# Optimization experiments

Hardware: AMD Instinct MI355X
Metric: run time of the kernel (lower is better)

## Reference

```python
import jax, jax.numpy as jnp
import numpy as np

N_EXPERTS = 8  # matches init n_experts


def _dispatch(x, expert_weights, top_experts, bias):
    """Faithful port of Experts.forward: sort tokens by expert, binned_gather
    into [E, capacity, d] with capacity-based token dropping, binned_scatter
    back weighted by expert_weights, then add bias. (The shown source never
    applies self.expert inside permute_and_compute, so the expert compute is
    identity; cond/mask are gathered then discarded and do not affect output.)"""
    b, n, d = x.shape
    top_k = top_experts.shape[-1]
    T = b * n * top_k
    # expert_capacity = int(top_k * tokens / n_experts)  (static)
    C = (top_k * b * n) // N_EXPERTS
    te = top_experts.reshape(-1).astype(jnp.int32)          # [T]
    w = expert_weights.reshape(-1)                           # [T]
    # ops.sort (stable radix sort over expert ids)
    order = jnp.argsort(te, stable=True)                     # indices [T]
    bin_ids = te[order]                                      # sorted expert ids
    # ops.histogram + inclusive_cumsum -> bin starts
    tpe = jnp.zeros((N_EXPERTS,), jnp.int32).at[te].add(1)   # tokens_per_expert
    starts = jnp.cumsum(tpe) - tpe                           # exclusive cumsum
    pos = jnp.arange(T, dtype=jnp.int32) - starts[bin_ids]   # position in bin
    valid = pos < C                                          # capacity drop
    slot = bin_ids * C + pos                                 # flat [E*C] slot
    tok = order // top_k                                     # source token row
    xf = x.reshape(-1, d)
    # binned_gather: [E*C, d], invalid entries routed to a dummy row
    gathered = (jnp.zeros((N_EXPERTS * C + 1, d), x.dtype)
                .at[jnp.where(valid, slot, N_EXPERTS * C)].set(xf[tok]))[:N_EXPERTS * C]
    # binned_scatter: out[tok] += w * gathered[slot] for valid entries
    wv = jnp.where(valid, w[order], jnp.zeros((), w.dtype))
    out = (jnp.zeros((b * n, d), x.dtype)
           .at[tok].add(wv[:, None] * gathered[jnp.where(valid, slot, 0)]))
    return out.reshape(b, n, d) + bias


def setup_inputs() -> dict:
    key = jax.random.key(0)
    k = jax.random.split(key, 6)
    b, n, d, dc, top_k = 4, 4096, 1024, 256, 2
    x = jax.random.normal(k[0], (b, n, d), jnp.float32)
    cond = jax.random.normal(k[1], (b, n, dc), jnp.float32)
    mask = jnp.ones((b, n), jnp.bool_)
    scores = jax.random.uniform(k[2], (b, n, N_EXPERTS), jnp.float32)
    expert_weights = jax.random.uniform(k[3], (b, n, top_k), jnp.float32)
    top_experts = jax.random.randint(k[4], (b, n, top_k), 0, N_EXPERTS, jnp.int32)
    bias = jax.random.normal(k[5], (d,), jnp.float32)
    return {"x": x, "cond": cond, "mask": mask, "scores": scores,
            "expert_weights": expert_weights, "top_experts": top_experts,
            "bias": bias}


def reference(x, cond, mask, scores, expert_weights, top_experts, bias):
    return _dispatch(x, expert_weights, top_experts, bias)
```

## Files before the change

### kernel.cpp

```cpp
#include <hip/hip_runtime.h>

#define N_EXPERTS 8
#define ROWS_PB 8
#define ENT_PB 16
typedef unsigned long long u64;
typedef float f32x4 __attribute__((ext_vector_type(4)));
typedef int i32x4 __attribute__((ext_vector_type(4)));

__device__ __forceinline__ void packed_add(u64& c0, u64& c1, int e) {
  if (e < 4) c0 += 1ull << (16 * e);
  else       c1 += 1ull << (16 * (e - 4));
}
__device__ __forceinline__ void packed_add_val(u64& c0, u64& c1, int e, int v) {
  if (e < 4) c0 += (u64)v << (16 * e);
  else       c1 += (u64)v << (16 * (e - 4));
}
__device__ __forceinline__ int packed_get(u64 c0, u64 c1, int e) {
  return (e < 4) ? (int)((c0 >> (16 * e)) & 0xFFFF)
                 : (int)((c1 >> (16 * (e - 4))) & 0xFFFF);
}

__global__ __launch_bounds__(256) void hist_kernel(
    const int* __restrict__ te, int* __restrict__ hist) {
  __shared__ u64 w0s[4], w1s[4];
  const int tid = threadIdx.x;
  const int lane = tid & 63, wid = tid >> 6;
  const int g = blockIdx.x * 256 + tid;
  const i32x4 v = reinterpret_cast<const i32x4*>(te)[g];

  u64 c0 = 0, c1 = 0;
  packed_add(c0, c1, v.x & 7);
  packed_add(c0, c1, v.y & 7);
  packed_add(c0, c1, v.z & 7);
  packed_add(c0, c1, v.w & 7);
#pragma unroll
  for (int m = 1; m < 64; m <<= 1) {
    c0 += __shfl_xor(c0, m);
    c1 += __shfl_xor(c1, m);
  }
  if (lane == 0) { w0s[wid] = c0; w1s[wid] = c1; }
  __syncthreads();
  if (tid < N_EXPERTS) {
    int s = 0;
#pragma unroll
    for (int ww = 0; ww < 4; ++ww) s += packed_get(w0s[ww], w1s[ww], tid);
    hist[blockIdx.x * N_EXPERTS + tid] = s;
  }
}

__global__ __launch_bounds__(256) void fused_kernel(
    const float* __restrict__ x, const int* __restrict__ te,
    const float* __restrict__ ew, const int* __restrict__ hist,
    const float* __restrict__ bias, float* __restrict__ out, int C) {
  __shared__ u64 w0s[4], w1s[4];
  __shared__ float scale_s[ROWS_PB];
  const int tid = threadIdx.x;
  const int lane = tid & 63, wid = tid >> 6;
  const int b = blockIdx.x;
  const int E0 = b * ENT_PB;
  const int sb = b >> 6;
  const int partial4 = 4 * (b & 63);

  const i32x4* __restrict__ te4 = reinterpret_cast<const i32x4*>(te);

  const f32x4* __restrict__ x4 =
      reinterpret_cast<const f32x4*>(x) + b * (ROWS_PB * 256);
  f32x4 xv0 = x4[0 * 256 + tid];
  f32x4 xv1 = x4[1 * 256 + tid];
  f32x4 xv2 = x4[2 * 256 + tid];
  f32x4 xv3 = x4[3 * 256 + tid];
  f32x4 xv4 = x4[4 * 256 + tid];
  f32x4 xv5 = x4[5 * 256 + tid];
  f32x4 xv6 = x4[6 * 256 + tid];
  f32x4 xv7 = x4[7 * 256 + tid];
  const f32x4 bv = reinterpret_cast<const f32x4*>(bias)[tid];

  u64 c0 = 0, c1 = 0;
  {
    const int bb = tid >> 3;
    if (bb < sb) packed_add_val(c0, c1, tid & 7, hist[tid]);
  }
  if (tid < partial4) {
    const i32x4 v = te4[sb * 256 + tid];
    packed_add(c0, c1, v.x & 7);
    packed_add(c0, c1, v.y & 7);
    packed_add(c0, c1, v.z & 7);
    packed_add(c0, c1, v.w & 7);
  }
#pragma unroll
  for (int m = 1; m < 64; m <<= 1) {
    c0 += __shfl_xor(c0, m);
    c1 += __shfl_xor(c1, m);
  }
  if (lane == 0) { w0s[wid] = c0; w1s[wid] = c1; }
  __syncthreads();

  if (tid == 0) {
    u64 p0 = w0s[0] + w0s[1] + w0s[2] + w0s[3];
    u64 p1 = w1s[0] + w1s[1] + w1s[2] + w1s[3];
    const f32x4* __restrict__ ew4 = reinterpret_cast<const f32x4*>(ew);
#pragma unroll
    for (int q = 0; q < 4; ++q) {
      const i32x4 v = te4[(E0 >> 2) + q];
      const f32x4 w = ew4[(E0 >> 2) + q];
      const int ee[4] = {v.x & 7, v.y & 7, v.z & 7, v.w & 7};
      const float wv[4] = {w.x, w.y, w.z, w.w};
      float s01 = 0.f, s23 = 0.f;
#pragma unroll
      for (int k = 0; k < 4; ++k) {
        const int e = ee[k];
        const int r = packed_get(p0, p1, e);
        packed_add(p0, p1, e);
        if (r < C) {
          if (k < 2) s01 += wv[k]; else s23 += wv[k];
        }
      }
      scale_s[q * 2 + 0] = s01;
      scale_s[q * 2 + 1] = s23;
    }
  }
  __syncthreads();

  f32x4* __restrict__ o4 = reinterpret_cast<f32x4*>(out) + b * (ROWS_PB * 256);
  {
    float s;
    f32x4 ov;
#define EMIT(K, XV)                                   \
    s = scale_s[K];                                   \
    ov = XV * s + bv;                                 \
    __builtin_nontemporal_store(ov, &o4[K * 256 + tid]);
    EMIT(0, xv0) EMIT(1, xv1) EMIT(2, xv2) EMIT(3, xv3)
    EMIT(4, xv4) EMIT(5, xv5) EMIT(6, xv6) EMIT(7, xv7)
#undef EMIT
  }
}

extern "C" void kernel_launch(void* const* d_in, const int* in_sizes, int n_in,
                              void* d_out, int out_size, void* d_ws,
                              size_t ws_size, hipStream_t stream) {
  const float* x    = (const float*)d_in[0];
  const float* ew   = (const float*)d_in[4];
  const int*   te   = (const int*)d_in[5];
  const float* bias = (const float*)d_in[6];
  float* out = (float*)d_out;
  int* hist = (int*)d_ws;

  const int T = in_sizes[5];
  const int C = T / N_EXPERTS;
  const int nblocks = (in_sizes[0] / 1024) / ROWS_PB;

  hist_kernel<<<32, 256, 0, stream>>>(te, hist);
  fused_kernel<<<nblocks, 256, 0, stream>>>(x, te, ew, hist, bias, out, C);
}
```

Baseline: 30.23 us.

## Fuse histogram into main kernel with cross-block flag-checked spin-wait

Removes the separate histogram kernel launch. The first nsb blocks of the main kernel compute per-superblock expert counts and publish them with a release atomic store, packed with a magic-XOR checksum. Consuming blocks spin with acquire loads until the checksum validates. This saves a launch and the inter-kernel gap, but it assumes producer blocks get scheduled, and it risks reading stale workspace from a previous call whose checksum is already valid.

```diff
diff --git a/kernel.cpp b/kernel.cpp
--- a/kernel.cpp
+++ b/kernel.cpp
@@ -3,7 +3,9 @@
 #define N_EXPERTS 8
 #define ROWS_PB 8
 #define ENT_PB 16
+#define MAGIC 0x9E3779B9u
 typedef unsigned long long u64;
+typedef unsigned int u32;
 typedef float f32x4 __attribute__((ext_vector_type(4)));
 typedef int i32x4 __attribute__((ext_vector_type(4)));
 
@@ -20,38 +22,10 @@
                  : (int)((c1 >> (16 * (e - 4))) & 0xFFFF);
 }
 
-__global__ __launch_bounds__(256) void hist_kernel(
-    const int* __restrict__ te, int* __restrict__ hist) {
-  __shared__ u64 w0s[4], w1s[4];
-  const int tid = threadIdx.x;
-  const int lane = tid & 63, wid = tid >> 6;
-  const int g = blockIdx.x * 256 + tid;
-  const i32x4 v = reinterpret_cast<const i32x4*>(te)[g];
-
-  u64 c0 = 0, c1 = 0;
-  packed_add(c0, c1, v.x & 7);
-  packed_add(c0, c1, v.y & 7);
-  packed_add(c0, c1, v.z & 7);
-  packed_add(c0, c1, v.w & 7);
-#pragma unroll
-  for (int m = 1; m < 64; m <<= 1) {
-    c0 += __shfl_xor(c0, m);
-    c1 += __shfl_xor(c1, m);
-  }
-  if (lane == 0) { w0s[wid] = c0; w1s[wid] = c1; }
-  __syncthreads();
-  if (tid < N_EXPERTS) {
-    int s = 0;
-#pragma unroll
-    for (int ww = 0; ww < 4; ++ww) s += packed_get(w0s[ww], w1s[ww], tid);
-    hist[blockIdx.x * N_EXPERTS + tid] = s;
-  }
-}
-
-__global__ __launch_bounds__(256) void fused_kernel(
+__global__ __launch_bounds__(256, 8) void fused_kernel(
     const float* __restrict__ x, const int* __restrict__ te,
-    const float* __restrict__ ew, const int* __restrict__ hist,
-    const float* __restrict__ bias, float* __restrict__ out, int C) {
+    const float* __restrict__ ew, const float* __restrict__ bias,
+    float* __restrict__ out, u64* __restrict__ h64, int C, int nsb) {
   __shared__ u64 w0s[4], w1s[4];
   __shared__ float scale_s[ROWS_PB];
   const int tid = threadIdx.x;
@@ -62,6 +36,31 @@
   const int partial4 = 4 * (b & 63);
 
   const i32x4* __restrict__ te4 = reinterpret_cast<const i32x4*>(te);
+
+  if (b < nsb) {
+    const i32x4 v = te4[b * 256 + tid];
+    u64 a0 = 0, a1 = 0;
+    packed_add(a0, a1, v.x & 7);
+    packed_add(a0, a1, v.y & 7);
+    packed_add(a0, a1, v.z & 7);
+    packed_add(a0, a1, v.w & 7);
+#pragma unroll
+    for (int m = 1; m < 64; m <<= 1) {
+      a0 += __shfl_xor(a0, m);
+      a1 += __shfl_xor(a1, m);
+    }
+    if (lane == 0) { w0s[wid] = a0; w1s[wid] = a1; }
+    __syncthreads();
+    if (tid < N_EXPERTS) {
+      int cnt = 0;
+#pragma unroll
+      for (int ww = 0; ww < 4; ++ww) cnt += packed_get(w0s[ww], w1s[ww], tid);
+      const u64 pk = ((u64)(((u32)cnt) ^ MAGIC) << 32) | (u32)cnt;
+      __hip_atomic_store(&h64[b * N_EXPERTS + tid], pk, __ATOMIC_RELEASE,
+                         __HIP_MEMORY_SCOPE_AGENT);
+    }
+    __syncthreads();
+  }
 
   const f32x4* __restrict__ x4 =
       reinterpret_cast<const f32x4*>(x) + b * (ROWS_PB * 256);
@@ -78,7 +77,17 @@
   u64 c0 = 0, c1 = 0;
   {
     const int bb = tid >> 3;
-    if (bb < sb) packed_add_val(c0, c1, tid & 7, hist[tid]);
+    if (bb < sb) {
+      u64 pk;
+      int guard = 0;
+      do {
+        pk = __hip_atomic_load(&h64[tid], __ATOMIC_ACQUIRE,
+                               __HIP_MEMORY_SCOPE_AGENT);
+        if ((u32)(pk >> 32) == (((u32)pk) ^ MAGIC)) break;
+        __builtin_amdgcn_s_sleep(2);
+      } while (++guard < (1 << 24));
+      packed_add_val(c0, c1, tid & 7, (int)(u32)pk);
+    }
   }
   if (tid < partial4) {
     const i32x4 v = te4[sb * 256 + tid];
@@ -143,12 +152,12 @@
   const int*   te   = (const int*)d_in[5];
   const float* bias = (const float*)d_in[6];
   float* out = (float*)d_out;
-  int* hist = (int*)d_ws;
+  u64* h64 = (u64*)d_ws;
 
   const int T = in_sizes[5];
   const int C = T / N_EXPERTS;
+  const int nsb = T / 1024;
   const int nblocks = (in_sizes[0] / 1024) / ROWS_PB;
 
-  hist_kernel<<<32, 256, 0, stream>>>(te, hist);
-  fused_kernel<<<nblocks, 256, 0, stream>>>(x, te, ew, hist, bias, out, C);
+  fused_kernel<<<nblocks, 256, 0, stream>>>(x, te, ew, bias, out, h64, C, nsb);
 }
```

After: 51.76 us. +71.2%, slower.

## Double rows per block and parallelize in-block rank computation across threads

Applied to the files above, without the earlier changes.

Each block now handles 16 rows instead of 8, which halves the grid and the per-block prefix/histogram overhead, and adds an occupancy hint of 4 blocks per CU. The serial single-thread loop that computed the in-bin rank of each top-k entry is replaced by 32 threads that each count earlier matching expert ids from shared memory and combine pairs with a shuffle. The larger block holds 16 float4 loads per thread in registers, which raises register pressure, and each block has a longer prefix section.

```diff
diff --git a/kernel.cpp b/kernel.cpp
--- a/kernel.cpp
+++ b/kernel.cpp
@@ -1,9 +1,10 @@
 #include <hip/hip_runtime.h>
 
 #define N_EXPERTS 8
-#define ROWS_PB 8
-#define ENT_PB 16
+#define ROWS_PB 16
+#define ENT_PB 32
 typedef unsigned long long u64;
+typedef unsigned int u32;
 typedef float f32x4 __attribute__((ext_vector_type(4)));
 typedef int i32x4 __attribute__((ext_vector_type(4)));
 
@@ -48,32 +49,40 @@
   }
 }
 
-__global__ __launch_bounds__(256) void fused_kernel(
+__global__ __launch_bounds__(256, 4) void fused_kernel(
     const float* __restrict__ x, const int* __restrict__ te,
     const float* __restrict__ ew, const int* __restrict__ hist,
     const float* __restrict__ bias, float* __restrict__ out, int C) {
   __shared__ u64 w0s[4], w1s[4];
+  __shared__ int ids_s[ENT_PB];
   __shared__ float scale_s[ROWS_PB];
   const int tid = threadIdx.x;
   const int lane = tid & 63, wid = tid >> 6;
   const int b = blockIdx.x;
   const int E0 = b * ENT_PB;
-  const int sb = b >> 6;
-  const int partial4 = 4 * (b & 63);
+  const int sb = b >> 5;
+  const int partial4 = 8 * (b & 31);
 
   const i32x4* __restrict__ te4 = reinterpret_cast<const i32x4*>(te);
 
   const f32x4* __restrict__ x4 =
       reinterpret_cast<const f32x4*>(x) + b * (ROWS_PB * 256);
-  f32x4 xv0 = x4[0 * 256 + tid];
-  f32x4 xv1 = x4[1 * 256 + tid];
-  f32x4 xv2 = x4[2 * 256 + tid];
-  f32x4 xv3 = x4[3 * 256 + tid];
-  f32x4 xv4 = x4[4 * 256 + tid];
-  f32x4 xv5 = x4[5 * 256 + tid];
-  f32x4 xv6 = x4[6 * 256 + tid];
-  f32x4 xv7 = x4[7 * 256 + tid];
+  f32x4 xv0 = x4[0 * 256 + tid],  xv1 = x4[1 * 256 + tid];
+  f32x4 xv2 = x4[2 * 256 + tid],  xv3 = x4[3 * 256 + tid];
+  f32x4 xv4 = x4[4 * 256 + tid],  xv5 = x4[5 * 256 + tid];
+  f32x4 xv6 = x4[6 * 256 + tid],  xv7 = x4[7 * 256 + tid];
+  f32x4 xv8 = x4[8 * 256 + tid],  xv9 = x4[9 * 256 + tid];
+  f32x4 xva = x4[10 * 256 + tid], xvb = x4[11 * 256 + tid];
+  f32x4 xvc = x4[12 * 256 + tid], xvd = x4[13 * 256 + tid];
+  f32x4 xve = x4[14 * 256 + tid], xvf = x4[15 * 256 + tid];
   const f32x4 bv = reinterpret_cast<const f32x4*>(bias)[tid];
+
+  int myid = 0;
+  float myw = 0.f;
+  if (tid < ENT_PB) {
+    myid = te[E0 + tid] & 7;
+    myw = ew[E0 + tid];
+  }
 
   u64 c0 = 0, c1 = 0;
   {
@@ -93,31 +102,19 @@
     c1 += __shfl_xor(c1, m);
   }
   if (lane == 0) { w0s[wid] = c0; w1s[wid] = c1; }
+  if (tid < ENT_PB) ids_s[tid] = myid;
   __syncthreads();
 
-  if (tid == 0) {
-    u64 p0 = w0s[0] + w0s[1] + w0s[2] + w0s[3];
-    u64 p1 = w1s[0] + w1s[1] + w1s[2] + w1s[3];
-    const f32x4* __restrict__ ew4 = reinterpret_cast<const f32x4*>(ew);
+  if (tid < ENT_PB) {
+    const u64 p0 = w0s[0] + w0s[1] + w0s[2] + w0s[3];
+    const u64 p1 = w1s[0] + w1s[1] + w1s[2] + w1s[3];
+    int r = packed_get(p0, p1, myid);
 #pragma unroll
-    for (int q = 0; q < 4; ++q) {
-      const i32x4 v = te4[(E0 >> 2) + q];
-      const f32x4 w = ew4[(E0 >> 2) + q];
-      const int ee[4] = {v.x & 7, v.y & 7, v.z & 7, v.w & 7};
-      const float wv[4] = {w.x, w.y, w.z, w.w};
-      float s01 = 0.f, s23 = 0.f;
-#pragma unroll
-      for (int k = 0; k < 4; ++k) {
-        const int e = ee[k];
-        const int r = packed_get(p0, p1, e);
-        packed_add(p0, p1, e);
-        if (r < C) {
-          if (k < 2) s01 += wv[k]; else s23 += wv[k];
-        }
-      }
-      scale_s[q * 2 + 0] = s01;
-      scale_s[q * 2 + 1] = s23;
-    }
+    for (int j = 0; j < ENT_PB - 1; ++j)
+      r += (j < tid) & (ids_s[j] == myid);
+    float contrib = (r < C) ? myw : 0.f;
+    const float pair = contrib + __shfl_xor(contrib, 1);
+    if ((tid & 1) == 0) scale_s[tid >> 1] = pair;
   }
   __syncthreads();
 
@@ -131,6 +128,8 @@
     __builtin_nontemporal_store(ov, &o4[K * 256 + tid]);
     EMIT(0, xv0) EMIT(1, xv1) EMIT(2, xv2) EMIT(3, xv3)
     EMIT(4, xv4) EMIT(5, xv5) EMIT(6, xv6) EMIT(7, xv7)
+    EMIT(8, xv8) EMIT(9, xv9) EMIT(10, xva) EMIT(11, xvb)
+    EMIT(12, xvc) EMIT(13, xvd) EMIT(14, xve) EMIT(15, xvf)
 #undef EMIT
   }
 }
```

Measured after the change: 30.50 us. Within noise of the previous version (+0.9%).
